# Kernel optimization log

Measured on AMD Instinct MI355X. Metric: run time of the kernel, lower is better.

The kernel has to match this reference:

```python
import jax, jax.numpy as jnp
import numpy as np

B, H, L, DK = 8, 8, 512, 64
LK, C = 512, 5


def setup_inputs() -> dict:
    key = jax.random.key(0)
    ks = jax.random.split(key, 6)
    d_in = LK * H * DK  # l_k * d_model
    return {
        "Q": jax.random.normal(ks[0], (B, H, L, DK), dtype=jnp.float32),
        "K": jax.random.normal(ks[1], (B, H, LK, DK), dtype=jnp.float32),
        # scale by 1/sqrt(fan_in) so softmax inputs are sane
        "W_proj": jax.random.normal(ks[2], (d_in, C), dtype=jnp.float32) / np.sqrt(d_in),
        "b_proj": jnp.zeros((C,), dtype=jnp.float32),
        "W_q": jax.random.normal(ks[3], (C, C), dtype=jnp.float32) / np.sqrt(C),
        "b_q": jnp.zeros((C,), dtype=jnp.float32),
        "W_k": jax.random.normal(ks[4], (C, C), dtype=jnp.float32) / np.sqrt(C),
        "b_k": jnp.zeros((C,), dtype=jnp.float32),
    }


def reference(Q, K, W_proj, b_proj, W_q, b_q, W_k, b_k):
    b, h, l, d_k = Q.shape
    l_k = K.shape[2]
    n_clusters = b_proj.shape[0]
    hd = h * d_k

    # cluster projections over flattened K
    ck_proj = K.reshape(b, -1) @ W_proj + b_proj            # (b, C)
    cluster_q = jax.nn.softmax(ck_proj @ W_q + b_q, axis=-1)  # (b, C)
    cluster_k = jax.nn.softmax(ck_proj @ W_k + b_k, axis=-1)  # (b, C)

    # Gaussian likelihood term (torch.std is unbiased -> ddof=1)
    mu = jnp.mean(cluster_q, axis=0)                         # (C,)
    sigma = jax.nn.softplus(jnp.std(cluster_k, axis=0, ddof=1))
    log_prob = (-0.5 * ((cluster_k - mu) / sigma) ** 2
                - jnp.log(sigma) - 0.5 * jnp.log(2.0 * jnp.pi))
    # CrossEntropyLoss with prob targets: mean_b(-sum target*log_softmax(input))
    ce = jnp.mean(-jnp.sum(cluster_q * jax.nn.log_softmax(cluster_q, axis=-1), axis=-1))
    loss = -jnp.mean(log_prob) + ce

    # cluster assignment per batch element
    inds = jnp.argmax(cluster_q, axis=-1)                    # (b,) in [0, C)

    # The original per-cluster loop with where(K_cluster != i+1, K_inds, 0) then
    # mean(dim=0)[0] reduces to: mean over batch of K_re[:,0,:] masked where
    # assignment != i+1, broadcast across l_k.
    K_re = K.reshape(b, l_k, hd)
    row0 = K_re[:, 0, :]                                     # (b, hd)
    keep = (inds[None, :] != (jnp.arange(n_clusters) + 1)[:, None]).astype(Q.dtype)  # (C, b)
    means = (keep @ row0) / b                                # (C, hd)

    # broadcast to (b, C, l_k, hd) then raw reshape to (b, h, C, l_k, d_k)
    cm = jnp.broadcast_to(means[None, :, None, :], (b, n_clusters, l_k, hd))
    cm = cm.reshape(b, h, n_clusters, l_k, d_k)

    scale = 1.0 / np.sqrt(d_k)
    scores_qk = jnp.einsum('bhqd,bhkd->bhqk', Q, K) * scale          # (b,h,l,l_k)
    scores_qc = jnp.einsum('bhqd,bhckd->bhcqk', Q, cm) * scale       # (b,h,C,l,l_k)
    # max over cat([qk, qc], dim=2) == elementwise max of qk and max_c qc
    final_score = jnp.maximum(scores_qk, jnp.max(scores_qc, axis=2))
    return final_score, loss
```

## Files before the change

### kernel.cpp

```cpp
#include <hip/hip_runtime.h>
#include <math.h>

#define NB 8
#define NH 8
#define SEQ 512
#define DK 64
#define NC 5
#define D_IN 262144
#define OUT_SCORE (NB*NH*SEQ*SEQ)
#define PROJ_BLOCKS 128

typedef short short8 __attribute__((ext_vector_type(8)));
typedef float f32x16 __attribute__((ext_vector_type(16)));

__device__ __forceinline__ short f2bf(float f) {
  unsigned u = __float_as_uint(f);
  u += 0x7fffu + ((u >> 16) & 1u);
  return (short)(u >> 16);
}
__device__ __forceinline__ short8 pack8(float4 a, float4 b) {
  short8 r;
  r[0] = f2bf(a.x); r[1] = f2bf(a.y); r[2] = f2bf(a.z); r[3] = f2bf(a.w);
  r[4] = f2bf(b.x); r[5] = f2bf(b.y); r[6] = f2bf(b.z); r[7] = f2bf(b.w);
  return r;
}

__global__ __launch_bounds__(256) void proj_kernel(const float* __restrict__ K,
                                                   const float* __restrict__ Wp,
                                                   float* __restrict__ part) {
  const float4* Wp4 = (const float4*)Wp;
  float acc[NB][NC];
#pragma unroll
  for (int b = 0; b < NB; ++b)
#pragma unroll
    for (int c = 0; c < NC; ++c) acc[b][c] = 0.f;

#pragma unroll
  for (int it = 0; it < 2; ++it) {
    int i4 = blockIdx.x * 512 + it * 256 + threadIdx.x;
    float w[20];
#pragma unroll
    for (int t = 0; t < 5; ++t) {
      float4 v = Wp4[i4 * 5 + t];
      w[4*t+0] = v.x; w[4*t+1] = v.y; w[4*t+2] = v.z; w[4*t+3] = v.w;
    }
#pragma unroll
    for (int b = 0; b < NB; ++b) {
      float4 kv = ((const float4*)(K + (size_t)b * D_IN))[i4];
      float ke[4] = {kv.x, kv.y, kv.z, kv.w};
#pragma unroll
      for (int e = 0; e < 4; ++e)
#pragma unroll
        for (int c = 0; c < NC; ++c)
          acc[b][c] = fmaf(ke[e], w[5*e + c], acc[b][c]);
    }
  }

  __shared__ float red[4][NB * NC];
  int wave = threadIdx.x >> 6;
  int lane = threadIdx.x & 63;
#pragma unroll
  for (int bc = 0; bc < NB * NC; ++bc) {
    float v = acc[bc / NC][bc % NC];
#pragma unroll
    for (int off = 32; off > 0; off >>= 1) v += __shfl_down(v, off);
    if (lane == 0) red[wave][bc] = v;
  }
  __syncthreads();
  if (threadIdx.x < NB * NC)
    part[blockIdx.x * (NB * NC) + threadIdx.x] =
        red[0][threadIdx.x] + red[1][threadIdx.x] +
        red[2][threadIdx.x] + red[3][threadIdx.x];
}

__global__ __launch_bounds__(256) void small_kernel(
    const float* __restrict__ K, const float* __restrict__ part,
    const float* __restrict__ bp, const float* __restrict__ Wq,
    const float* __restrict__ bq, const float* __restrict__ Wk,
    const float* __restrict__ bk, float* __restrict__ means,
    float* __restrict__ loss_out) {
  __shared__ float colsum[NB * NC];
  __shared__ float cq[NB][NC], ckk[NB][NC], ce_sh[NB];
  __shared__ int inds[NB];
  int t = threadIdx.x;
  if (t < NB * NC) {
    float s = 0.f;
    for (int i = 0; i < PROJ_BLOCKS; ++i) s += part[i * (NB * NC) + t];
    colsum[t] = s;
  }
  __syncthreads();
  if (t < NB) {
    float cp[NC], zq[NC], zk[NC];
#pragma unroll
    for (int c = 0; c < NC; ++c) cp[c] = colsum[t * NC + c] + bp[c];
#pragma unroll
    for (int c = 0; c < NC; ++c) { zq[c] = bq[c]; zk[c] = bk[c]; }
#pragma unroll
    for (int j = 0; j < NC; ++j)
#pragma unroll
      for (int c = 0; c < NC; ++c) {
        zq[c] = fmaf(cp[j], Wq[j * NC + c], zq[c]);
        zk[c] = fmaf(cp[j], Wk[j * NC + c], zk[c]);
      }
    float m = zq[0];
#pragma unroll
    for (int c = 1; c < NC; ++c) m = fmaxf(m, zq[c]);
    float e[NC], s = 0.f;
#pragma unroll
    for (int c = 0; c < NC; ++c) { e[c] = expf(zq[c] - m); s += e[c]; }
    float inv = 1.f / s;
    float p[NC];
#pragma unroll
    for (int c = 0; c < NC; ++c) { p[c] = e[c] * inv; cq[t][c] = p[c]; }
    int am = 0; float bv = p[0];
#pragma unroll
    for (int c = 1; c < NC; ++c) if (p[c] > bv) { bv = p[c]; am = c; }
    inds[t] = am;
    float se = 0.f;
#pragma unroll
    for (int c = 0; c < NC; ++c) se += expf(p[c] - bv);
    float lse = bv + logf(se);
    float ceb = 0.f;
#pragma unroll
    for (int c = 0; c < NC; ++c) ceb -= p[c] * (p[c] - lse);
    ce_sh[t] = ceb;
    m = zk[0];
#pragma unroll
    for (int c = 1; c < NC; ++c) m = fmaxf(m, zk[c]);
    s = 0.f;
#pragma unroll
    for (int c = 0; c < NC; ++c) { e[c] = expf(zk[c] - m); s += e[c]; }
    inv = 1.f / s;
#pragma unroll
    for (int c = 0; c < NC; ++c) ckk[t][c] = e[c] * inv;
  }
  __syncthreads();
  if (t == 0) {
    float mu[NC];
#pragma unroll
    for (int c = 0; c < NC; ++c) {
      float sm = 0.f;
      for (int b = 0; b < NB; ++b) sm += cq[b][c];
      mu[c] = sm * 0.125f;
    }
    float loss_lp = 0.f;
#pragma unroll
    for (int c = 0; c < NC; ++c) {
      float sm = 0.f;
      for (int b = 0; b < NB; ++b) sm += ckk[b][c];
      float mk = sm * 0.125f;
      float var = 0.f;
      for (int b = 0; b < NB; ++b) {
        float d = ckk[b][c] - mk;
        var += d * d;
      }
      var *= (1.f / 7.f);
      float sd = sqrtf(var);
      float sigma = log1pf(expf(sd));
      float ls = logf(sigma);
      for (int b = 0; b < NB; ++b) {
        float z = (ckk[b][c] - mu[c]) / sigma;
        loss_lp += -0.5f * z * z - ls - 0.91893853320467274f;
      }
    }
    float ce = 0.f;
    for (int b = 0; b < NB; ++b) ce += ce_sh[b];
    ce *= 0.125f;
    loss_out[0] = -(loss_lp / 40.f) + ce;
  }
  __syncthreads();
  for (int idx = t; idx < NC * 512; idx += 256) {
    int c = idx >> 9, j = idx & 511;
    float sm = 0.f;
#pragma unroll
    for (int b = 0; b < NB; ++b)
      if (inds[b] != c + 1) sm += K[(size_t)b * D_IN + j];
    means[idx] = sm * 0.125f;
  }
}

#define LDSTRIDE 72
__global__ __launch_bounds__(256) void score_kernel(const float* __restrict__ Q,
                                                    const float* __restrict__ K,
                                                    const float* __restrict__ means,
                                                    float* __restrict__ out) {
  __shared__ short Qs[128 * LDSTRIDE];
  __shared__ short Ks[128 * LDSTRIDE];
  __shared__ float qcbuf[4 * 64 * 10];

  const int bh = blockIdx.x;
  const int h  = bh & 7;
  const int qblk = blockIdx.y << 7;
  const int kblk = blockIdx.z << 7;
  const int tid = threadIdx.x;
  const int w = tid >> 6, lane = tid & 63;
  const int lo5 = lane & 31, hi = lane >> 5;
  const int wq = (w >> 1) << 6;
  const int wk = (w & 1) << 6;

  const float* Qg = Q + (size_t)bh * (SEQ * DK) + (size_t)qblk * DK;
  const float* Kg = K + (size_t)bh * (SEQ * DK) + (size_t)kblk * DK;

#pragma unroll
  for (int i = 0; i < 4; ++i) {
    int f8 = i * 256 + tid;
    int row = f8 >> 3, c8 = f8 & 7;
    const float4* qp = (const float4*)(Qg + row * DK + c8 * 8);
    const float4* kp = (const float4*)(Kg + row * DK + c8 * 8);
    *(short8*)&Qs[row * LDSTRIDE + c8 * 8] = pack8(qp[0], qp[1]);
    *(short8*)&Ks[row * LDSTRIDE + c8 * 8] = pack8(kp[0], kp[1]);
  }

  const int cmin = (5 * h) >> 3;
  const int cmax = (5 * h + 4) >> 3;
  short8 mfrag[4];
#pragma unroll
  for (int s = 0; s < 4; ++s) {
    float4 a = {0.f, 0.f, 0.f, 0.f}, b = {0.f, 0.f, 0.f, 0.f};
    if (lo5 < 16) {
      int c = (lo5 < 8) ? cmin : cmax;
      const float* mp = means + c * 512 + (lo5 & 7) * 64 + s * 16 + hi * 8;
      a = *(const float4*)mp;
      b = *(const float4*)(mp + 4);
    }
    mfrag[s] = pack8(a, b);
  }

  __syncthreads();

  f32x16 zero;
#pragma unroll
  for (int x = 0; x < 16; ++x) zero[x] = 0.f;

  f32x16 acc00 = zero, acc01 = zero, acc10 = zero, acc11 = zero;
  f32x16 aq0 = zero, aq1 = zero;
#pragma unroll
  for (int s = 0; s < 4; ++s) {
    int co = s * 16 + hi * 8;
    short8 a0 = *(const short8*)&Qs[(wq + lo5)      * LDSTRIDE + co];
    short8 a1 = *(const short8*)&Qs[(wq + 32 + lo5) * LDSTRIDE + co];
    short8 b0 = *(const short8*)&Ks[(wk + lo5)      * LDSTRIDE + co];
    short8 b1 = *(const short8*)&Ks[(wk + 32 + lo5) * LDSTRIDE + co];
    acc00 = __builtin_amdgcn_mfma_f32_32x32x16_bf16(a0, b0, acc00, 0, 0, 0);
    acc01 = __builtin_amdgcn_mfma_f32_32x32x16_bf16(a0, b1, acc01, 0, 0, 0);
    acc10 = __builtin_amdgcn_mfma_f32_32x32x16_bf16(a1, b0, acc10, 0, 0, 0);
    acc11 = __builtin_amdgcn_mfma_f32_32x32x16_bf16(a1, b1, acc11, 0, 0, 0);
    aq0   = __builtin_amdgcn_mfma_f32_32x32x16_bf16(mfrag[s], a0, aq0, 0, 0, 0);
    aq1   = __builtin_amdgcn_mfma_f32_32x32x16_bf16(mfrag[s], a1, aq1, 0, 0, 0);
  }

  {
    int qb0 = w * 640 + lo5 * 10 + 4 * hi;
    float2 p;
    p.x = fmaxf(aq0[0], aq0[4]) * 0.125f;
    p.y = fmaxf(aq0[1], aq0[5]) * 0.125f;
    *(float2*)&qcbuf[qb0] = p;
    p.x = fmaxf(aq0[2], aq0[6]) * 0.125f;
    p.y = fmaxf(aq0[3], aq0[7]) * 0.125f;
    *(float2*)&qcbuf[qb0 + 2] = p;
    int qb1 = qb0 + 320;
    p.x = fmaxf(aq1[0], aq1[4]) * 0.125f;
    p.y = fmaxf(aq1[1], aq1[5]) * 0.125f;
    *(float2*)&qcbuf[qb1] = p;
    p.x = fmaxf(aq1[2], aq1[6]) * 0.125f;
    p.y = fmaxf(aq1[3], aq1[7]) * 0.125f;
    *(float2*)&qcbuf[qb1 + 2] = p;
  }

  float* ob = out + (size_t)bh * (SEQ * SEQ);
  const int kc0 = kblk + wk + lo5;
  const int r = lo5 & 7;
  const int qcb = w * 640 + r;
#pragma unroll
  for (int g = 0; g < 4; ++g) {
#pragma unroll
    for (int e = 0; e < 4; ++e) {
      int reg = 4 * g + e;
      int ql = e + 8 * g + 4 * hi;
      float qc0 = qcbuf[qcb + ql * 10];
      float qc1 = qcbuf[qcb + (ql + 32) * 10];
      int qrow = qblk + wq + ql;
      ob[(size_t)qrow * SEQ + kc0]             = fmaxf(acc00[reg] * 0.125f, qc0);
      ob[(size_t)qrow * SEQ + kc0 + 32]        = fmaxf(acc01[reg] * 0.125f, qc0);
      ob[(size_t)(qrow + 32) * SEQ + kc0]      = fmaxf(acc10[reg] * 0.125f, qc1);
      ob[(size_t)(qrow + 32) * SEQ + kc0 + 32] = fmaxf(acc11[reg] * 0.125f, qc1);
    }
  }
}

extern "C" void kernel_launch(void* const* d_in, const int* in_sizes, int n_in,
                              void* d_out, int out_size, void* d_ws, size_t ws_size,
                              hipStream_t stream) {
  const float* Q  = (const float*)d_in[0];
  const float* K  = (const float*)d_in[1];
  const float* Wp = (const float*)d_in[2];
  const float* bp = (const float*)d_in[3];
  const float* Wq = (const float*)d_in[4];
  const float* bq = (const float*)d_in[5];
  const float* Wk = (const float*)d_in[6];
  const float* bk = (const float*)d_in[7];
  float* out = (float*)d_out;

  float* part  = (float*)d_ws;
  float* means = part + 8192;

  proj_kernel<<<PROJ_BLOCKS, 256, 0, stream>>>(K, Wp, part);
  small_kernel<<<1, 256, 0, stream>>>(K, part, bp, Wq, bq, Wk, bk, means,
                                      out + OUT_SCORE);
  dim3 grid(64, 4, 4);
  score_kernel<<<grid, 256, 0, stream>>>(Q, K, means, out);
}
```

Before: 130.9 us.

## Split projection across batch halves and alias score LDS buffer onto Q tile

The projection kernel now launches 512 blocks, each handling one float4 column slice for four batch rows, where it previously used 128 blocks each covering two slices for all eight rows. This lowers registers per thread and raises parallelism for the bandwidth-bound K·W_proj reduction, at the cost of loading W_proj twice and giving the single-block reduce kernel more partials to sum. Separately, the score kernel reuses the Q shared-memory tile for its qc buffer, with an added barrier, which cuts LDS usage and may improve occupancy.

```diff
diff --git a/kernel.cpp b/kernel.cpp
--- a/kernel.cpp
+++ b/kernel.cpp
@@ -8,7 +8,7 @@
 #define NC 5
 #define D_IN 262144
 #define OUT_SCORE (NB*NH*SEQ*SEQ)
-#define PROJ_BLOCKS 128
+#define PROJ_BLOCKS 512
 
 typedef short short8 __attribute__((ext_vector_type(8)));
 typedef float f32x16 __attribute__((ext_vector_type(16)));
@@ -28,47 +28,44 @@
 __global__ __launch_bounds__(256) void proj_kernel(const float* __restrict__ K,
                                                    const float* __restrict__ Wp,
                                                    float* __restrict__ part) {
+  const int bsel = blockIdx.x >> 8;
+  const int i4 = (blockIdx.x & 255) * 256 + threadIdx.x;
   const float4* Wp4 = (const float4*)Wp;
-  float acc[NB][NC];
-#pragma unroll
-  for (int b = 0; b < NB; ++b)
+  float w[20];
+#pragma unroll
+  for (int t = 0; t < 5; ++t) {
+    float4 v = Wp4[i4 * 5 + t];
+    w[4*t+0] = v.x; w[4*t+1] = v.y; w[4*t+2] = v.z; w[4*t+3] = v.w;
+  }
+  float acc[4][NC];
+#pragma unroll
+  for (int b = 0; b < 4; ++b)
 #pragma unroll
     for (int c = 0; c < NC; ++c) acc[b][c] = 0.f;
-
-#pragma unroll
-  for (int it = 0; it < 2; ++it) {
-    int i4 = blockIdx.x * 512 + it * 256 + threadIdx.x;
-    float w[20];
-#pragma unroll
-    for (int t = 0; t < 5; ++t) {
-      float4 v = Wp4[i4 * 5 + t];
-      w[4*t+0] = v.x; w[4*t+1] = v.y; w[4*t+2] = v.z; w[4*t+3] = v.w;
-    }
-#pragma unroll
-    for (int b = 0; b < NB; ++b) {
-      float4 kv = ((const float4*)(K + (size_t)b * D_IN))[i4];
-      float ke[4] = {kv.x, kv.y, kv.z, kv.w};
-#pragma unroll
-      for (int e = 0; e < 4; ++e)
-#pragma unroll
-        for (int c = 0; c < NC; ++c)
-          acc[b][c] = fmaf(ke[e], w[5*e + c], acc[b][c]);
-    }
-  }
-
-  __shared__ float red[4][NB * NC];
+#pragma unroll
+  for (int b = 0; b < 4; ++b) {
+    float4 kv = ((const float4*)(K + (size_t)(bsel * 4 + b) * D_IN))[i4];
+    float ke[4] = {kv.x, kv.y, kv.z, kv.w};
+#pragma unroll
+    for (int e = 0; e < 4; ++e)
+#pragma unroll
+      for (int c = 0; c < NC; ++c)
+        acc[b][c] = fmaf(ke[e], w[5*e + c], acc[b][c]);
+  }
+
+  __shared__ float red[4][4 * NC];
   int wave = threadIdx.x >> 6;
   int lane = threadIdx.x & 63;
 #pragma unroll
-  for (int bc = 0; bc < NB * NC; ++bc) {
+  for (int bc = 0; bc < 4 * NC; ++bc) {
     float v = acc[bc / NC][bc % NC];
 #pragma unroll
     for (int off = 32; off > 0; off >>= 1) v += __shfl_down(v, off);
     if (lane == 0) red[wave][bc] = v;
   }
   __syncthreads();
-  if (threadIdx.x < NB * NC)
-    part[blockIdx.x * (NB * NC) + threadIdx.x] =
+  if (threadIdx.x < 4 * NC)
+    part[blockIdx.x * (4 * NC) + threadIdx.x] =
         red[0][threadIdx.x] + red[1][threadIdx.x] +
         red[2][threadIdx.x] + red[3][threadIdx.x];
 }
@@ -84,8 +81,11 @@
   __shared__ int inds[NB];
   int t = threadIdx.x;
   if (t < NB * NC) {
+    int b = t / NC, c = t % NC;
+    int base = (b >> 2) * 256;
+    int slot = (b & 3) * NC + c;
     float s = 0.f;
-    for (int i = 0; i < PROJ_BLOCKS; ++i) s += part[i * (NB * NC) + t];
+    for (int i = 0; i < 256; ++i) s += part[(base + i) * (4 * NC) + slot];
     colsum[t] = s;
   }
   __syncthreads();
@@ -186,7 +186,7 @@
                                                     float* __restrict__ out) {
   __shared__ short Qs[128 * LDSTRIDE];
   __shared__ short Ks[128 * LDSTRIDE];
-  __shared__ float qcbuf[4 * 64 * 10];
+  float* qcbuf = (float*)Qs;
 
   const int bh = blockIdx.x;
   const int h  = bh & 7;
@@ -248,6 +248,8 @@
     aq0   = __builtin_amdgcn_mfma_f32_32x32x16_bf16(mfrag[s], a0, aq0, 0, 0, 0);
     aq1   = __builtin_amdgcn_mfma_f32_32x32x16_bf16(mfrag[s], a1, aq1, 0, 0, 0);
   }
+
+  __syncthreads();
 
   {
     int qb0 = w * 640 + lo5 * 10 + 4 * hi;
@@ -302,7 +304,7 @@
   float* out = (float*)d_out;
 
   float* part  = (float*)d_ws;
-  float* means = part + 8192;
+  float* means = part + PROJ_BLOCKS * 20;
 
   proj_kernel<<<PROJ_BLOCKS, 256, 0, stream>>>(K, Wp, part);
   small_kernel<<<1, 256, 0, stream>>>(K, part, bp, Wq, bq, Wk, bk, means,
```

Result: no change. 133.0 us (+1.6%).
